# Kernel optimization log

Measured on AMD Instinct MI355X. Metric: run time of the kernel, lower is better.

The kernel has to match this reference:

```python
import jax, jax.numpy as jnp
import numpy as np

EMBED, HEADS, WIN = 512, 1, 16  # head_dim == EMBED since HEADS == 1
B, S = 4, 2048


def setup_inputs() -> dict:
    key = jax.random.key(0)
    ks = jax.random.split(key, 9)
    sc = 1.0 / np.sqrt(EMBED)
    return {
        "x": jax.random.normal(ks[0], (B, S, EMBED), dtype=jnp.float32),
        "Wq": jax.random.normal(ks[1], (EMBED, EMBED), dtype=jnp.float32) * sc,
        "bq": jax.random.normal(ks[2], (EMBED,), dtype=jnp.float32) * 0.01,
        "Wk": jax.random.normal(ks[3], (EMBED, EMBED), dtype=jnp.float32) * sc,
        "bk": jax.random.normal(ks[4], (EMBED,), dtype=jnp.float32) * 0.01,
        "Wv": jax.random.normal(ks[5], (EMBED, EMBED), dtype=jnp.float32) * sc,
        "bv": jax.random.normal(ks[6], (EMBED,), dtype=jnp.float32) * 0.01,
        "Wo": jax.random.normal(ks[7], (EMBED, EMBED), dtype=jnp.float32) * sc,
        "bo": jax.random.normal(ks[8], (EMBED,), dtype=jnp.float32) * 0.01,
    }


def reference(x, Wq, bq, Wk, bk, Wv, bv, Wo, bo):
    Bsz, Sq, E = x.shape
    w = WIN
    W = 2 * w + 1  # window span
    # Pad sequence with zeros (as F.pad in the original); the Linear bias is
    # applied to padded positions too (linear(0) = bias), matching torch.
    xp = jnp.pad(x, ((0, 0), (w, w), (0, 0)))  # [B, S+2w, E]
    Qp = xp @ Wq.T + bq
    Kp = xp @ Wk.T + bk
    Vp = xp @ Wv.T + bv
    # Original energy: einsum('bswhd,bswhd->bswh') -> dot of Q and K at the
    # SAME window slot, so it collapses to a per-position scalar, then gathered.
    scale = 1.0 / float(E) ** 0.5  # head_dim == E since heads == 1
    e = jnp.sum(Qp * Kp, axis=-1) * scale  # [B, S+2w]
    idx = jnp.arange(Sq)[:, None] + jnp.arange(W)[None, :]  # [S, W] into padded
    ew = e[:, idx]  # [B, S, W]
    attn = jax.nn.softmax(ew, axis=2)  # softmax over window dim
    Vw = Vp[:, idx]  # [B, S, W, E]
    out = jnp.einsum('bsw,bswe->bse', attn, Vw)  # [B, S, E]
    return out @ Wo.T + bo
```

## Files before the change

### kernel.cpp

```cpp
#include <hip/hip_runtime.h>
#include <stdint.h>

#define SEQ 2048
#define BATCH 4
#define EMB 512
#define MTOT (BATCH * SEQ)
#define WIN 16
#define WINDOW 33

typedef uint32_t u32;
typedef unsigned short u16;
typedef __attribute__((ext_vector_type(8))) __bf16 bf16x8;
typedef __attribute__((ext_vector_type(4))) float f32x4;
typedef __attribute__((ext_vector_type(4))) u16 u16x4;
typedef __attribute__((ext_vector_type(8))) u16 u16x8;

__device__ __forceinline__ u16 f2bf(float f) {
  u32 u = __builtin_bit_cast(u32, f);
  u = (u + 0x7fffu + ((u >> 16) & 1u)) >> 16;
  return (u16)u;
}
__device__ __forceinline__ float bf2f(u16 v) {
  return __builtin_bit_cast(float, (u32)v << 16);
}
__device__ __forceinline__ void gload16(void* lds, const void* g) {
  __builtin_amdgcn_global_load_lds((const __attribute__((address_space(1))) u32*)g,
                                   (__attribute__((address_space(3))) u32*)lds, 16, 0, 0);
}
__device__ __forceinline__ void drain_stage() {
  asm volatile("s_waitcnt vmcnt(0) lgkmcnt(0)" ::: "memory");
}

__global__ void __launch_bounds__(256) prep5(
    const float* __restrict__ x, const float* __restrict__ Wq, const float* __restrict__ Wk,
    const float* __restrict__ Wv, const float* __restrict__ Wo,
    const float* __restrict__ bq, const float* __restrict__ bk,
    const float* __restrict__ bv, const float* __restrict__ bo,
    u16* __restrict__ xb, u16* __restrict__ WqT, u16* __restrict__ WkT,
    u16* __restrict__ Wob, u16* __restrict__ WvT,
    float* __restrict__ cvec, float* __restrict__ bc, float* __restrict__ econst) {
  __shared__ float sm[32][33];
  int b = blockIdx.x, t = threadIdx.x;
  if (b < 512) {
    for (u32 i = b * 256 + t; i < (u32)(MTOT * EMB / 4); i += 512 * 256) {
      float4 v = reinterpret_cast<const float4*>(x)[i];
      u16x4 o; o.x = f2bf(v.x); o.y = f2bf(v.y); o.z = f2bf(v.z); o.w = f2bf(v.w);
      reinterpret_cast<u16x4*>(xb)[i] = o;
    }
  } else if (b < 1280 && !(b >= 1024 && b < 1280)) {
    bool isQ = b < 768;
    int tb = (b - 512) & 255;
    const float* S = isQ ? Wq : Wk;
    u16* D = isQ ? WqT : WkT;
    int ti = tb >> 4, tj = tb & 15;
    int lr = t >> 5, lc = t & 31;
#pragma unroll
    for (int rr = 0; rr < 32; rr += 8)
      sm[rr + lr][lc] = S[(size_t)(ti * 32 + rr + lr) * EMB + tj * 32 + lc];
    __syncthreads();
    int jr = t >> 3, dc = (t & 7) * 4;
    u16x4 o;
#pragma unroll
    for (int c = 0; c < 4; ++c) o[c] = f2bf(sm[dc + c][jr]);
    *reinterpret_cast<u16x4*>(D + (size_t)(tj * 32 + jr) * EMB + ti * 32 + dc) = o;
  } else if (b < 1280) {
    int cb = b - 1024;
    int i = (cb * 256 + t) * 4;
    float4 v = *reinterpret_cast<const float4*>(Wo + i);
    u16x4 o; o.x = f2bf(v.x); o.y = f2bf(v.y); o.z = f2bf(v.z); o.w = f2bf(v.w);
    *reinterpret_cast<u16x4*>(Wob + i) = o;
  } else if (b < 1536) {
    int tb = b - 1280;
    int ti = tb >> 4, tj = tb & 15;
    int lr = t >> 5, lc = t & 31;
#pragma unroll
    for (int rr = 0; rr < 32; rr += 8)
      sm[rr + lr][lc] = Wv[(size_t)(ti * 32 + rr + lr) * EMB + tj * 32 + lc];
    __syncthreads();
    int jr = t >> 3, dc = (t & 7) * 4;
    u16x4 o;
#pragma unroll
    for (int c = 0; c < 4; ++c) o[c] = f2bf(sm[dc + c][jr]);
    *reinterpret_cast<u16x4*>(WvT + (size_t)(tj * 32 + jr) * EMB + ti * 32 + dc) = o;
  } else if (b < 1544) {
    float* sh = &sm[0][0];
    int cb = b - 1536;
    int ii = t >> 2, di = t & 3;
    int i = cb * 64 + ii;
    float s = 0.f;
    for (int d = di * 128; d < di * 128 + 128; ++d)
      s += Wq[(size_t)d * EMB + i] * bk[d] + Wk[(size_t)d * EMB + i] * bq[d];
    sh[t] = s;
    __syncthreads();
    if (di == 0) cvec[i] = sh[t] + sh[t + 1] + sh[t + 2] + sh[t + 3];
  } else if (b < 1552) {
    float* sh = &sm[0][0];
    int cb = b - 1544;
    int ii = t >> 2, di = t & 3;
    int i = cb * 64 + ii;
    float s = 0.f;
    for (int d = di * 128; d < di * 128 + 128; ++d)
      s += Wo[(size_t)i * EMB + d] * bv[d];
    sh[t] = s;
    __syncthreads();
    if (di == 0) bc[i] = sh[t] + sh[t + 1] + sh[t + 2] + sh[t + 3] + bo[i];
  } else {
    float* sh = &sm[0][0];
    float s = bq[t] * bk[t] + bq[t + 256] * bk[t + 256];
    sh[t] = s;
    __syncthreads();
    for (int st = 128; st > 0; st >>= 1) {
      if (t < st) sh[t] += sh[t + st];
      __syncthreads();
    }
    if (t == 0) *econst = sh[0];
  }
}

__device__ __forceinline__ void bt_tile64(
    const u16* __restrict__ Arows, const u16* __restrict__ Brows, u16* __restrict__ C,
    int i0, int j0, int t, char* smem) {
  u16* AL = (u16*)smem;
  u16* BL = (u16*)(smem + 4096);
  int wave = t >> 6, lane = t & 63;
  int wr = wave >> 1, wc = wave & 1;
  int fr = lane & 15, fq = lane >> 4;
  f32x4 acc[2][2] = {};
  for (int kt = 0; kt < 16; ++kt) {
    __syncthreads();
    int kb = kt * 32;
    int row = t >> 2, col8 = (t & 3) * 8;
    gload16(AL + (size_t)t * 8, Arows + (size_t)(i0 + row) * EMB + kb + col8);
    gload16(BL + (size_t)t * 8, Brows + (size_t)(j0 + row) * EMB + kb + col8);
    drain_stage();
    __syncthreads();
    bf16x8 af[2], bfv[2];
#pragma unroll
    for (int m = 0; m < 2; ++m)
      af[m] = *reinterpret_cast<const bf16x8*>(&AL[(wr * 32 + m * 16 + fr) * 32 + fq * 8]);
#pragma unroll
    for (int n = 0; n < 2; ++n)
      bfv[n] = *reinterpret_cast<const bf16x8*>(&BL[(wc * 32 + n * 16 + fr) * 32 + fq * 8]);
#pragma unroll
    for (int m = 0; m < 2; ++m)
#pragma unroll
      for (int n = 0; n < 2; ++n)
        acc[m][n] = __builtin_amdgcn_mfma_f32_16x16x32_bf16(af[m], bfv[n], acc[m][n], 0, 0, 0);
  }
#pragma unroll
  for (int m = 0; m < 2; ++m) {
    int wave2 = t >> 6;
    int wr2 = wave2 >> 1, wc2 = wave2 & 1;
    int fr2 = (t & 63) & 15, fq2 = (t & 63) >> 4;
#pragma unroll
    for (int n = 0; n < 2; ++n)
#pragma unroll
      for (int r = 0; r < 4; ++r)
        C[(size_t)(i0 + wr2 * 32 + m * 16 + fq2 * 4 + r) * EMB + j0 + wc2 * 32 + n * 16 + fr2] =
            f2bf(acc[m][n][r]);
  }
}

__global__ void __launch_bounds__(256) gemm_atm(
    const u16* __restrict__ WkT, const u16* __restrict__ WqT, u16* __restrict__ Atm) {
  __shared__ __align__(16) char smem[8192];
  int b = blockIdx.x;
  bt_tile64(WkT, WqT, Atm, (b >> 3) * 64, (b & 7) * 64, threadIdx.x, smem);
}

__global__ void __launch_bounds__(256) gemm_ewc(
    const u16* __restrict__ xb, const u16* __restrict__ Atm,
    const float* __restrict__ x, const float* __restrict__ cvec,
    float* __restrict__ e_part,
    const u16* __restrict__ Wob, const u16* __restrict__ WvT, u16* __restrict__ Wcb) {
  __shared__ __align__(16) char smem[12288];
  int b = blockIdx.x;
  int t = threadIdx.x;
  if (b >= 512) {
    bt_tile64(Wob, WvT, Wcb, ((b - 512) >> 3) * 64, ((b - 512) & 7) * 64, t, smem);
    return;
  }
  u16* At2 = (u16*)smem;
  u16* Bt2 = (u16*)(smem + 4096);
  int wg = ((b & 7) << 6) + (b >> 3);
  int bx = wg >> 2, by = wg & 3;
  int wave = t >> 6, lane = t & 63;
  int wr = wave >> 1, wc = wave & 1;
  int fr = lane & 15, fq = lane >> 4;
  int m0 = bx * 64, n0 = by * 128;
  f32x4 acc[2][4] = {};
  for (int kt = 0; kt < EMB / 32; ++kt) {
    __syncthreads();
    int kb = kt * 32;
    {
      int row = t >> 2, col = (t & 3) * 8;
      gload16(At2 + (size_t)t * 8, xb + (size_t)(m0 + row) * EMB + kb + col);
    }
#pragma unroll
    for (int it = 0; it < 2; ++it) {
      int chunk = t + it * 256;
      int row = chunk >> 2, col = (chunk & 3) * 8;
      gload16(Bt2 + (size_t)(wave * 64 + it * 256) * 8, Atm + (size_t)(n0 + row) * EMB + kb + col);
    }
    drain_stage();
    __syncthreads();
    bf16x8 af[2], bfv[4];
#pragma unroll
    for (int m = 0; m < 2; ++m)
      af[m] = *reinterpret_cast<const bf16x8*>(&At2[(wr * 32 + m * 16 + fr) * 32 + fq * 8]);
#pragma unroll
    for (int n = 0; n < 4; ++n)
      bfv[n] = *reinterpret_cast<const bf16x8*>(&Bt2[(wc * 64 + n * 16 + fr) * 32 + fq * 8]);
#pragma unroll
    for (int m = 0; m < 2; ++m)
#pragma unroll
      for (int n = 0; n < 4; ++n)
        acc[m][n] = __builtin_amdgcn_mfma_f32_16x16x32_bf16(af[m], bfv[n], acc[m][n], 0, 0, 0);
  }
  float cv[4];
#pragma unroll
  for (int n = 0; n < 4; ++n) cv[n] = cvec[n0 + wc * 64 + n * 16 + fr];
  int slot = by * 2 + wc;
#pragma unroll
  for (int m = 0; m < 2; ++m) {
#pragma unroll
    for (int r = 0; r < 4; ++r) {
      int row = m0 + wr * 32 + m * 16 + fq * 4 + r;
      float p = 0.f;
#pragma unroll
      for (int n = 0; n < 4; ++n) {
        int col = n0 + wc * 64 + n * 16 + fr;
        p += (acc[m][n][r] + cv[n]) * x[(size_t)row * EMB + col];
      }
      p += __shfl_xor(p, 1);
      p += __shfl_xor(p, 2);
      p += __shfl_xor(p, 4);
      p += __shfl_xor(p, 8);
      if (fr == 0) e_part[(size_t)slot * MTOT + row] = p;
    }
  }
}

__global__ void __launch_bounds__(256) window4(
    const u16* __restrict__ xb, const float* __restrict__ e_part,
    const float* __restrict__ econst_p, u16* __restrict__ y) {
  __shared__ u16 Xt[48 * EMB];
  __shared__ float eloc[48];
  __shared__ float w[16][WINDOW];
  int b = blockIdx.x;
  int swz = ((b & 7) << 6) + (b >> 3);
  int bb = swz >> 7;
  int s0 = (swz & 127) * 16;
  int t = threadIdx.x;
  u16x8 stg[12];
#pragma unroll
  for (int i = 0; i < 12; ++i) {
    int chunk = t + i * 256;
    int row = chunk >> 6;
    int c8 = (chunk & 63) * 8;
    int n = s0 + row - WIN;
    if (n >= 0 && n < SEQ)
      stg[i] = *reinterpret_cast<const u16x8*>(xb + (size_t)(bb * SEQ + n) * EMB + c8);
    else
      stg[i] = (u16x8){0, 0, 0, 0, 0, 0, 0, 0};
  }
#pragma unroll
  for (int i = 0; i < 12; ++i) {
    int chunk = t + i * 256;
    int row = chunk >> 6;
    int c8 = (chunk & 63) * 8;
    *reinterpret_cast<u16x8*>(&Xt[(size_t)row * EMB + c8]) = stg[i];
  }
  const float scale = 0.044194173824159216f;
  float ec = *econst_p;
  if (t < 48) {
    int n = s0 + t - WIN;
    float raw = 0.f;
    if (n >= 0 && n < SEQ) {
      size_t idx = (size_t)bb * SEQ + n;
#pragma unroll
      for (int p = 0; p < 8; ++p) raw += e_part[(size_t)p * MTOT + idx];
    }
    eloc[t] = scale * (raw + ec);
  }
  __syncthreads();
  if (t < 16) {
    float ev[WINDOW];
    float mx = -1e30f;
#pragma unroll
    for (int j = 0; j < WINDOW; ++j) { ev[j] = eloc[t + j]; mx = fmaxf(mx, ev[j]); }
    float sum = 0.f;
#pragma unroll
    for (int j = 0; j < WINDOW; ++j) { float ex = __expf(ev[j] - mx); ev[j] = ex; sum += ex; }
    float inv = 1.f / sum;
#pragma unroll
    for (int j = 0; j < WINDOW; ++j) w[t][j] = ev[j] * inv;
  }
  __syncthreads();
  int cg = t & 63;
  int slg = t >> 6;
  int d0 = cg * 8;
  float oacc[4][8] = {};
  for (int ri = 0; ri < 36; ++ri) {
    int r = slg * 4 + ri;
    u16x8 v = *reinterpret_cast<const u16x8*>(&Xt[(size_t)r * EMB + d0]);
    float vf[8];
#pragma unroll
    for (int c = 0; c < 8; ++c) vf[c] = bf2f(v[c]);
#pragma unroll
    for (int q = 0; q < 4; ++q) {
      int j = ri - q;
      if (j >= 0 && j < WINDOW) {
        float wt = w[slg * 4 + q][j];
#pragma unroll
        for (int c = 0; c < 8; ++c) oacc[q][c] += wt * vf[c];
      }
    }
  }
#pragma unroll
  for (int q = 0; q < 4; ++q) {
    u16x8 o;
#pragma unroll
    for (int c = 0; c < 8; ++c) o[c] = f2bf(oacc[q][c]);
    *reinterpret_cast<u16x8*>(&y[(size_t)(bb * SEQ + s0 + slg * 4 + q) * EMB + d0]) = o;
  }
}

__global__ void __launch_bounds__(256) gemm_o(
    const u16* __restrict__ y, const u16* __restrict__ Wcb,
    const float* __restrict__ bc, float* __restrict__ out) {
  __shared__ u16 At2[64 * 32];
  __shared__ u16 Bt2[128 * 32];
  int b = blockIdx.x;
  int wg = ((b & 7) << 6) + (b >> 3);
  int bx = wg >> 2, by = wg & 3;
  int t = threadIdx.x;
  int wave = t >> 6, lane = t & 63;
  int wr = wave >> 1, wc = wave & 1;
  int fr = lane & 15, fq = lane >> 4;
  int m0 = bx * 64, n0 = by * 128;
  f32x4 acc[2][4] = {};
  for (int kt = 0; kt < EMB / 32; ++kt) {
    __syncthreads();
    int kb = kt * 32;
    {
      int row = t >> 2, col = (t & 3) * 8;
      gload16(At2 + (size_t)t * 8, y + (size_t)(m0 + row) * EMB + kb + col);
    }
#pragma unroll
    for (int it = 0; it < 2; ++it) {
      int chunk = t + it * 256;
      int row = chunk >> 2, col = (chunk & 3) * 8;
      gload16(Bt2 + (size_t)(wave * 64 + it * 256) * 8, Wcb + (size_t)(n0 + row) * EMB + kb + col);
    }
    drain_stage();
    __syncthreads();
    bf16x8 af[2], bfv[4];
#pragma unroll
    for (int m = 0; m < 2; ++m)
      af[m] = *reinterpret_cast<const bf16x8*>(&At2[(wr * 32 + m * 16 + fr) * 32 + fq * 8]);
#pragma unroll
    for (int n = 0; n < 4; ++n)
      bfv[n] = *reinterpret_cast<const bf16x8*>(&Bt2[(wc * 64 + n * 16 + fr) * 32 + fq * 8]);
#pragma unroll
    for (int m = 0; m < 2; ++m)
#pragma unroll
      for (int n = 0; n < 4; ++n)
        acc[m][n] = __builtin_amdgcn_mfma_f32_16x16x32_bf16(af[m], bfv[n], acc[m][n], 0, 0, 0);
  }
  float bcv[4];
#pragma unroll
  for (int n = 0; n < 4; ++n) bcv[n] = bc[n0 + wc * 64 + n * 16 + fr];
#pragma unroll
  for (int m = 0; m < 2; ++m)
#pragma unroll
    for (int n = 0; n < 4; ++n) {
      int col = n0 + wc * 64 + n * 16 + fr;
#pragma unroll
      for (int r = 0; r < 4; ++r) {
        int row = m0 + wr * 32 + m * 16 + fq * 4 + r;
        out[(size_t)row * EMB + col] = acc[m][n][r] + bcv[n];
      }
    }
}

extern "C" void kernel_launch(void* const* d_in, const int* in_sizes, int n_in,
                              void* d_out, int out_size, void* d_ws, size_t ws_size,
                              hipStream_t stream) {
  const float* x  = (const float*)d_in[0];
  const float* Wq = (const float*)d_in[1];
  const float* bq = (const float*)d_in[2];
  const float* Wk = (const float*)d_in[3];
  const float* bk = (const float*)d_in[4];
  const float* Wv = (const float*)d_in[5];
  const float* bv = (const float*)d_in[6];
  const float* Wo = (const float*)d_in[7];
  const float* bo = (const float*)d_in[8];
  float* out = (float*)d_out;

  char* ws = (char*)d_ws;
  u16* xb       = (u16*)(ws);
  u16* y        = (u16*)(ws + (8u << 20));
  u16* WqT      = (u16*)(ws + (16u << 20));
  u16* WkT      = (u16*)(ws + (16u << 20) + (512u << 10));
  u16* Wob      = (u16*)(ws + (16u << 20) + (1024u << 10));
  u16* WvT      = (u16*)(ws + (16u << 20) + (1536u << 10));
  u16* Atm      = (u16*)(ws + (16u << 20) + (2048u << 10));
  u16* Wcb      = (u16*)(ws + (16u << 20) + (2560u << 10));
  float* e_part = (float*)(ws + (16u << 20) + (3072u << 10));
  float* cvec   = (float*)(ws + (16u << 20) + (3328u << 10));
  float* bc     = (float*)(ws + (16u << 20) + (3330u << 10));
  float* econst = (float*)(ws + (16u << 20) + (3332u << 10));

  prep5<<<1553, 256, 0, stream>>>(x, Wq, Wk, Wv, Wo, bq, bk, bv, bo,
                                  xb, WqT, WkT, Wob, WvT, cvec, bc, econst);
  gemm_atm<<<64, 256, 0, stream>>>(WkT, WqT, Atm);
  gemm_ewc<<<576, 256, 0, stream>>>(xb, Atm, x, cvec, e_part, Wob, WvT, Wcb);
  window4<<<512, 256, 0, stream>>>(xb, e_part, econst, y);
  gemm_o<<<512, 256, 0, stream>>>(y, Wcb, bc, out);
}
```

Baseline: 68.28 us.

## Fuse weight-product GEMMs into prep kernel, reading fp32 weights directly

The small weight-product GEMMs (Wk^T·Wq and Wo·Wv) move into the prep kernel. Each tile loads fp32 weights, converts them to bf16 and transposes them into LDS on the fly, so the separate bf16 transposed copies of Wq, Wk, Wv and Wo are no longer written. This removes one kernel launch (gemm_atm) and the extra transpose passes, and gemm_e now only computes energies. The cost is scalar strided LDS stores with possible bank conflicts, plus the weight GEMMs now running alongside the x conversion inside one launch.

```diff
diff --git a/kernel.cpp b/kernel.cpp
--- a/kernel.cpp
+++ b/kernel.cpp
@@ -31,15 +31,14 @@
   asm volatile("s_waitcnt vmcnt(0) lgkmcnt(0)" ::: "memory");
 }
 
-__global__ void __launch_bounds__(256) prep5(
+__global__ void __launch_bounds__(256) prep6(
     const float* __restrict__ x, const float* __restrict__ Wq, const float* __restrict__ Wk,
     const float* __restrict__ Wv, const float* __restrict__ Wo,
     const float* __restrict__ bq, const float* __restrict__ bk,
     const float* __restrict__ bv, const float* __restrict__ bo,
-    u16* __restrict__ xb, u16* __restrict__ WqT, u16* __restrict__ WkT,
-    u16* __restrict__ Wob, u16* __restrict__ WvT,
+    u16* __restrict__ xb, u16* __restrict__ Atm, u16* __restrict__ Wcb,
     float* __restrict__ cvec, float* __restrict__ bc, float* __restrict__ econst) {
-  __shared__ float sm[32][33];
+  __shared__ __align__(16) char smem[8192];
   int b = blockIdx.x, t = threadIdx.x;
   if (b < 512) {
     for (u32 i = b * 256 + t; i < (u32)(MTOT * EMB / 4); i += 512 * 256) {
@@ -47,44 +46,74 @@
       u16x4 o; o.x = f2bf(v.x); o.y = f2bf(v.y); o.z = f2bf(v.z); o.w = f2bf(v.w);
       reinterpret_cast<u16x4*>(xb)[i] = o;
     }
-  } else if (b < 1280 && !(b >= 1024 && b < 1280)) {
-    bool isQ = b < 768;
-    int tb = (b - 512) & 255;
-    const float* S = isQ ? Wq : Wk;
-    u16* D = isQ ? WqT : WkT;
-    int ti = tb >> 4, tj = tb & 15;
-    int lr = t >> 5, lc = t & 31;
-#pragma unroll
-    for (int rr = 0; rr < 32; rr += 8)
-      sm[rr + lr][lc] = S[(size_t)(ti * 32 + rr + lr) * EMB + tj * 32 + lc];
-    __syncthreads();
-    int jr = t >> 3, dc = (t & 7) * 4;
-    u16x4 o;
-#pragma unroll
-    for (int c = 0; c < 4; ++c) o[c] = f2bf(sm[dc + c][jr]);
-    *reinterpret_cast<u16x4*>(D + (size_t)(tj * 32 + jr) * EMB + ti * 32 + dc) = o;
-  } else if (b < 1280) {
-    int cb = b - 1024;
-    int i = (cb * 256 + t) * 4;
-    float4 v = *reinterpret_cast<const float4*>(Wo + i);
-    u16x4 o; o.x = f2bf(v.x); o.y = f2bf(v.y); o.z = f2bf(v.z); o.w = f2bf(v.w);
-    *reinterpret_cast<u16x4*>(Wob + i) = o;
-  } else if (b < 1536) {
-    int tb = b - 1280;
-    int ti = tb >> 4, tj = tb & 15;
-    int lr = t >> 5, lc = t & 31;
-#pragma unroll
-    for (int rr = 0; rr < 32; rr += 8)
-      sm[rr + lr][lc] = Wv[(size_t)(ti * 32 + rr + lr) * EMB + tj * 32 + lc];
-    __syncthreads();
-    int jr = t >> 3, dc = (t & 7) * 4;
-    u16x4 o;
-#pragma unroll
-    for (int c = 0; c < 4; ++c) o[c] = f2bf(sm[dc + c][jr]);
-    *reinterpret_cast<u16x4*>(WvT + (size_t)(tj * 32 + jr) * EMB + ti * 32 + dc) = o;
-  } else if (b < 1544) {
-    float* sh = &sm[0][0];
-    int cb = b - 1536;
+  } else if (b < 640) {
+    bool isAtm = b < 576;
+    int tb = isAtm ? (b - 512) : (b - 576);
+    int i0 = (tb >> 3) * 64, j0 = (tb & 7) * 64;
+    u16* AL = (u16*)smem;
+    u16* BL = (u16*)(smem + 4096);
+    int wave = t >> 6, lane = t & 63;
+    int wr = wave >> 1, wc = wave & 1;
+    int fr = lane & 15, fq = lane >> 4;
+    f32x4 acc[2][2] = {};
+    for (int kt = 0; kt < 16; ++kt) {
+      __syncthreads();
+      int kb = kt * 32;
+      if (isAtm) {
+#pragma unroll
+        for (int p = 0; p < 2; ++p) {
+          int idx = t + p * 256;
+          int dd = idx >> 4, c4 = (idx & 15) * 4;
+          float4 FA = *reinterpret_cast<const float4*>(Wk + (size_t)(kb + dd) * EMB + i0 + c4);
+          float4 FB = *reinterpret_cast<const float4*>(Wq + (size_t)(kb + dd) * EMB + j0 + c4);
+#pragma unroll
+          for (int j = 0; j < 4; ++j) {
+            AL[(c4 + j) * 32 + dd] = f2bf(((const float*)&FA)[j]);
+            BL[(c4 + j) * 32 + dd] = f2bf(((const float*)&FB)[j]);
+          }
+        }
+      } else {
+#pragma unroll
+        for (int p = 0; p < 2; ++p) {
+          int idx = t + p * 256;
+          int row = idx >> 3, c4 = (idx & 7) * 4;
+          float4 FA = *reinterpret_cast<const float4*>(Wo + (size_t)(i0 + row) * EMB + kb + c4);
+          u16x4 oa; oa.x = f2bf(FA.x); oa.y = f2bf(FA.y); oa.z = f2bf(FA.z); oa.w = f2bf(FA.w);
+          *reinterpret_cast<u16x4*>(&AL[row * 32 + c4]) = oa;
+          int dd = idx >> 4, cc4 = (idx & 15) * 4;
+          float4 FB = *reinterpret_cast<const float4*>(Wv + (size_t)(kb + dd) * EMB + j0 + cc4);
+#pragma unroll
+          for (int j = 0; j < 4; ++j)
+            BL[(cc4 + j) * 32 + dd] = f2bf(((const float*)&FB)[j]);
+        }
+      }
+      drain_stage();
+      __syncthreads();
+      bf16x8 af[2], bfv[2];
+#pragma unroll
+      for (int m = 0; m < 2; ++m)
+        af[m] = *reinterpret_cast<const bf16x8*>(&AL[(wr * 32 + m * 16 + fr) * 32 + fq * 8]);
+#pragma unroll
+      for (int n = 0; n < 2; ++n)
+        bfv[n] = *reinterpret_cast<const bf16x8*>(&BL[(wc * 32 + n * 16 + fr) * 32 + fq * 8]);
+#pragma unroll
+      for (int m = 0; m < 2; ++m)
+#pragma unroll
+        for (int n = 0; n < 2; ++n)
+          acc[m][n] = __builtin_amdgcn_mfma_f32_16x16x32_bf16(af[m], bfv[n], acc[m][n], 0, 0, 0);
+    }
+    u16* C = isAtm ? Atm : Wcb;
+#pragma unroll
+    for (int m = 0; m < 2; ++m)
+#pragma unroll
+      for (int n = 0; n < 2; ++n)
+#pragma unroll
+        for (int r = 0; r < 4; ++r)
+          C[(size_t)(i0 + wr * 32 + m * 16 + fq * 4 + r) * EMB + j0 + wc * 32 + n * 16 + fr] =
+              f2bf(acc[m][n][r]);
+  } else if (b < 648) {
+    float* sh = (float*)smem;
+    int cb = b - 640;
     int ii = t >> 2, di = t & 3;
     int i = cb * 64 + ii;
     float s = 0.f;
@@ -93,9 +122,9 @@
     sh[t] = s;
     __syncthreads();
     if (di == 0) cvec[i] = sh[t] + sh[t + 1] + sh[t + 2] + sh[t + 3];
-  } else if (b < 1552) {
-    float* sh = &sm[0][0];
-    int cb = b - 1544;
+  } else if (b < 656) {
+    float* sh = (float*)smem;
+    int cb = b - 648;
     int ii = t >> 2, di = t & 3;
     int i = cb * 64 + ii;
     float s = 0.f;
@@ -105,7 +134,7 @@
     __syncthreads();
     if (di == 0) bc[i] = sh[t] + sh[t + 1] + sh[t + 2] + sh[t + 3] + bo[i];
   } else {
-    float* sh = &sm[0][0];
+    float* sh = (float*)smem;
     float s = bq[t] * bk[t] + bq[t + 256] * bk[t + 256];
     sh[t] = s;
     __syncthreads();
@@ -117,73 +146,16 @@
   }
 }
 
-__device__ __forceinline__ void bt_tile64(
-    const u16* __restrict__ Arows, const u16* __restrict__ Brows, u16* __restrict__ C,
-    int i0, int j0, int t, char* smem) {
-  u16* AL = (u16*)smem;
-  u16* BL = (u16*)(smem + 4096);
-  int wave = t >> 6, lane = t & 63;
-  int wr = wave >> 1, wc = wave & 1;
-  int fr = lane & 15, fq = lane >> 4;
-  f32x4 acc[2][2] = {};
-  for (int kt = 0; kt < 16; ++kt) {
-    __syncthreads();
-    int kb = kt * 32;
-    int row = t >> 2, col8 = (t & 3) * 8;
-    gload16(AL + (size_t)t * 8, Arows + (size_t)(i0 + row) * EMB + kb + col8);
-    gload16(BL + (size_t)t * 8, Brows + (size_t)(j0 + row) * EMB + kb + col8);
-    drain_stage();
-    __syncthreads();
-    bf16x8 af[2], bfv[2];
-#pragma unroll
-    for (int m = 0; m < 2; ++m)
-      af[m] = *reinterpret_cast<const bf16x8*>(&AL[(wr * 32 + m * 16 + fr) * 32 + fq * 8]);
-#pragma unroll
-    for (int n = 0; n < 2; ++n)
-      bfv[n] = *reinterpret_cast<const bf16x8*>(&BL[(wc * 32 + n * 16 + fr) * 32 + fq * 8]);
-#pragma unroll
-    for (int m = 0; m < 2; ++m)
-#pragma unroll
-      for (int n = 0; n < 2; ++n)
-        acc[m][n] = __builtin_amdgcn_mfma_f32_16x16x32_bf16(af[m], bfv[n], acc[m][n], 0, 0, 0);
-  }
-#pragma unroll
-  for (int m = 0; m < 2; ++m) {
-    int wave2 = t >> 6;
-    int wr2 = wave2 >> 1, wc2 = wave2 & 1;
-    int fr2 = (t & 63) & 15, fq2 = (t & 63) >> 4;
-#pragma unroll
-    for (int n = 0; n < 2; ++n)
-#pragma unroll
-      for (int r = 0; r < 4; ++r)
-        C[(size_t)(i0 + wr2 * 32 + m * 16 + fq2 * 4 + r) * EMB + j0 + wc2 * 32 + n * 16 + fr2] =
-            f2bf(acc[m][n][r]);
-  }
-}
-
-__global__ void __launch_bounds__(256) gemm_atm(
-    const u16* __restrict__ WkT, const u16* __restrict__ WqT, u16* __restrict__ Atm) {
-  __shared__ __align__(16) char smem[8192];
-  int b = blockIdx.x;
-  bt_tile64(WkT, WqT, Atm, (b >> 3) * 64, (b & 7) * 64, threadIdx.x, smem);
-}
-
-__global__ void __launch_bounds__(256) gemm_ewc(
+__global__ void __launch_bounds__(256) gemm_e(
     const u16* __restrict__ xb, const u16* __restrict__ Atm,
     const float* __restrict__ x, const float* __restrict__ cvec,
-    float* __restrict__ e_part,
-    const u16* __restrict__ Wob, const u16* __restrict__ WvT, u16* __restrict__ Wcb) {
-  __shared__ __align__(16) char smem[12288];
+    float* __restrict__ e_part) {
+  __shared__ u16 At2[64 * 32];
+  __shared__ u16 Bt2[128 * 32];
   int b = blockIdx.x;
-  int t = threadIdx.x;
-  if (b >= 512) {
-    bt_tile64(Wob, WvT, Wcb, ((b - 512) >> 3) * 64, ((b - 512) & 7) * 64, t, smem);
-    return;
-  }
-  u16* At2 = (u16*)smem;
-  u16* Bt2 = (u16*)(smem + 4096);
   int wg = ((b & 7) << 6) + (b >> 3);
   int bx = wg >> 2, by = wg & 3;
+  int t = threadIdx.x;
   int wave = t >> 6, lane = t & 63;
   int wr = wave >> 1, wc = wave & 1;
   int fr = lane & 15, fq = lane >> 4;
@@ -401,21 +373,16 @@
   char* ws = (char*)d_ws;
   u16* xb       = (u16*)(ws);
   u16* y        = (u16*)(ws + (8u << 20));
-  u16* WqT      = (u16*)(ws + (16u << 20));
-  u16* WkT      = (u16*)(ws + (16u << 20) + (512u << 10));
-  u16* Wob      = (u16*)(ws + (16u << 20) + (1024u << 10));
-  u16* WvT      = (u16*)(ws + (16u << 20) + (1536u << 10));
-  u16* Atm      = (u16*)(ws + (16u << 20) + (2048u << 10));
-  u16* Wcb      = (u16*)(ws + (16u << 20) + (2560u << 10));
-  float* e_part = (float*)(ws + (16u << 20) + (3072u << 10));
-  float* cvec   = (float*)(ws + (16u << 20) + (3328u << 10));
-  float* bc     = (float*)(ws + (16u << 20) + (3330u << 10));
-  float* econst = (float*)(ws + (16u << 20) + (3332u << 10));
-
-  prep5<<<1553, 256, 0, stream>>>(x, Wq, Wk, Wv, Wo, bq, bk, bv, bo,
-                                  xb, WqT, WkT, Wob, WvT, cvec, bc, econst);
-  gemm_atm<<<64, 256, 0, stream>>>(WkT, WqT, Atm);
-  gemm_ewc<<<576, 256, 0, stream>>>(xb, Atm, x, cvec, e_part, Wob, WvT, Wcb);
+  u16* Atm      = (u16*)(ws + (16u << 20));
+  u16* Wcb      = (u16*)(ws + (16u << 20) + (512u << 10));
+  float* e_part = (float*)(ws + (16u << 20) + (1024u << 10));
+  float* cvec   = (float*)(ws + (16u << 20) + (1280u << 10));
+  float* bc     = (float*)(ws + (16u << 20) + (1282u << 10));
+  float* econst = (float*)(ws + (16u << 20) + (1284u << 10));
+
+  prep6<<<657, 256, 0, stream>>>(x, Wq, Wk, Wv, Wo, bq, bk, bv, bo,
+                                 xb, Atm, Wcb, cvec, bc, econst);
+  gemm_e<<<512, 256, 0, stream>>>(xb, Atm, x, cvec, e_part);
   window4<<<512, 256, 0, stream>>>(xb, e_part, econst, y);
   gemm_o<<<512, 256, 0, stream>>>(y, Wcb, bc, out);
 }
```

Result: faster. 66.49 us (-2.6%).
